# Optimization experiments

Hardware: AMD Instinct MI355X
Metric: run time of the kernel (lower is better)

The kernel has to match this reference:

```python
import jax, jax.numpy as jnp
import numpy as np

H = 2048      # hidden_size
NH = 16       # num_heads
HD = H // NH  # head_dim
B, T = 2, 2048


def setup_inputs() -> dict:
    key = jax.random.key(0)
    ks = jax.random.split(key, 5)
    s = 1.0 / np.sqrt(H)
    return {
        "x": jax.random.normal(ks[0], (B, T, H), dtype=jnp.float32),
        "wq": jax.random.normal(ks[1], (H, H), dtype=jnp.float32) * s,
        "bq": jnp.zeros((H,), dtype=jnp.float32),
        "wk": jax.random.normal(ks[2], (H, H), dtype=jnp.float32) * s,
        "bk": jnp.zeros((H,), dtype=jnp.float32),
        "wv": jax.random.normal(ks[3], (H, H), dtype=jnp.float32) * s,
        "bv": jnp.zeros((H,), dtype=jnp.float32),
        "wo": jax.random.normal(ks[4], (H, H), dtype=jnp.float32) * s,
        "bo": jnp.zeros((H,), dtype=jnp.float32),
    }


def reference(x, wq, bq, wk, bk, wv, bv, wo, bo):
    Bx, Tx, C = x.shape
    # projections (torch Linear: x @ W.T + b)
    q = x @ wq.T + bq
    k = x @ wk.T + bk
    v = x @ wv.T + bv
    # [B, T, H] -> [B, NH, T, HD]
    q = q.reshape(Bx, Tx, NH, HD).transpose(0, 2, 1, 3)
    k = k.reshape(Bx, Tx, NH, HD).transpose(0, 2, 1, 3)
    v = v.reshape(Bx, Tx, NH, HD).transpose(0, 2, 1, 3)
    scale = 1.0 / np.sqrt(HD).astype(np.float32)
    scores = jnp.einsum('bhqd,bhkd->bhqk', q, k) * scale  # [B, NH, T, T]
    causal = jnp.tril(jnp.ones((Tx, Tx), dtype=bool))
    scores = jnp.where(causal[None, None], scores, -jnp.inf)
    attn = jax.nn.softmax(scores, axis=-1)
    out = jnp.einsum('bhqk,bhkd->bhqd', attn, v)  # [B, NH, T, HD]
    out = out.transpose(0, 2, 1, 3).reshape(Bx, Tx, C)
    return out @ wo.T + bo
```

## Files before the change

### kernel.cpp

```cpp
#include <hip/hip_runtime.h>
#include <stdint.h>

constexpr int H_  = 2048;
constexpr int NH_ = 16;
constexpr int HD_ = 128;
constexpr int B_  = 2;
constexpr int T_  = 2048;
constexpr int M_  = B_ * T_;

typedef unsigned short u16;
typedef __bf16 bf16x8 __attribute__((ext_vector_type(8)));
typedef float  f32x4  __attribute__((ext_vector_type(4)));

constexpr float C1_ = 0.08838834764831845f * 1.4426950408889634f;

template <int N> struct IC { static constexpr int value = N; };

__device__ __forceinline__ u16 f2bf(float f) {
  uint32_t u = __builtin_bit_cast(uint32_t, f);
  u += 0x7fffu + ((u >> 16) & 1u);
  return (u16)(u >> 16);
}

__device__ __forceinline__ uint32_t cvtpk(float lo, float hi) {
  uint32_t r;
  asm("v_cvt_pk_bf16_f32 %0, %1, %2" : "=v"(r) : "v"(lo), "v"(hi));
  return r;
}

__device__ __forceinline__ void gload_lds16(const void* g, void* lds) {
  auto gp = (const __attribute__((address_space(1))) uint32_t*)(uintptr_t)g;
  auto lp = (__attribute__((address_space(3))) uint32_t*)(uint32_t)(uintptr_t)lds;
  __builtin_amdgcn_global_load_lds(gp, lp, 16, 0, 0);
}

__device__ __forceinline__ f32x4 mfma16(bf16x8 a, bf16x8 b, f32x4 c) {
  return __builtin_amdgcn_mfma_f32_16x16x32_bf16(a, b, c, 0, 0, 0);
}

__global__ __launch_bounds__(512) void cvt5_kernel(
    const float4* __restrict__ x,  const float4* __restrict__ wq,
    const float4* __restrict__ wk, const float4* __restrict__ wv,
    const float4* __restrict__ wo, ushort4* __restrict__ dst) {
  const int bid = blockIdx.x, tid = threadIdx.x;
  const float4* src;
  size_t idx, dof;
  if (bid < 4096) {
    src = x; idx = (size_t)bid * 512 + tid; dof = 0;
  } else {
    int w = (bid - 4096) >> 11;
    int r = (bid - 4096) & 2047;
    idx = (size_t)r * 512 + tid;
    dof = 2097152u + (size_t)w * 1048576u;
    src = (w == 0) ? wq : (w == 1) ? wk : (w == 2) ? wv : wo;
  }
  float4 v = src[idx];
  ushort4 o;
  o.x = f2bf(v.x); o.y = f2bf(v.y); o.z = f2bf(v.z); o.w = f2bf(v.w);
  dst[dof + idx] = o;
}

__device__ __forceinline__ void gemm_core(const u16* __restrict__ A,
                                          const u16* __restrict__ Bm,
                                          const float* __restrict__ bias,
                                          void* __restrict__ Cout,
                                          int bid, int outmode, float oscale) {
  __shared__ u16 As[2][128 * 64];
  __shared__ u16 Bs[2][128 * 64];
  constexpr int Mg = M_, Ng = H_, Kg = H_;
  const int tid = threadIdx.x;
  const int wave = tid >> 6, lane = tid & 63, l15 = lane & 15, lhi = lane >> 4;
  const int tm = bid % (Mg >> 7), tn = bid / (Mg >> 7);
  const int m0 = tm << 7, n0 = tn << 7;
  const int wr = wave >> 1, wc = wave & 1;
  const int NT = Kg >> 6;

  f32x4 acc[4][4] = {};

  auto stage = [&](int kt, int buf) {
#pragma unroll
    for (int is = 0; is < 4; ++is) {
      int o  = is * 4096 + tid * 16;
      int row = o >> 7;
      int sw  = o ^ (((o >> 7) & 7) << 4);
      int c8  = (sw >> 4) & 7;
      gload_lds16(A + (size_t)(m0 + row) * Kg + kt * 64 + c8 * 8,
                  &As[buf][0] + (is * 2048 + wave * 512));
      gload_lds16(Bm + (size_t)(n0 + row) * Kg + kt * 64 + c8 * 8,
                  &Bs[buf][0] + (is * 2048 + wave * 512));
    }
  };

  stage(0, 0);
  int cur = 0;
  for (int kt = 0; kt < NT; ++kt) {
    if (kt + 1 < NT) {
      stage(kt + 1, cur ^ 1);
      asm volatile("s_waitcnt vmcnt(8)" ::: "memory");
    } else {
      asm volatile("s_waitcnt vmcnt(0)" ::: "memory");
    }
    __builtin_amdgcn_s_barrier();
    asm volatile("" ::: "memory");
#pragma unroll
    for (int kk = 0; kk < 2; ++kk) {
      bf16x8 af[4], bfr[4];
#pragma unroll
      for (int mi = 0; mi < 4; ++mi) {
        int row = wr * 64 + mi * 16 + l15;
        int ob  = (row * 128 + kk * 64 + lhi * 16) ^ ((row & 7) << 4);
        af[mi] = *(const bf16x8*)((const char*)&As[cur][0] + ob);
      }
#pragma unroll
      for (int ni = 0; ni < 4; ++ni) {
        int row = wc * 64 + ni * 16 + l15;
        int ob  = (row * 128 + kk * 64 + lhi * 16) ^ ((row & 7) << 4);
        bfr[ni] = *(const bf16x8*)((const char*)&Bs[cur][0] + ob);
      }
#pragma unroll
      for (int mi = 0; mi < 4; ++mi)
#pragma unroll
        for (int ni = 0; ni < 4; ++ni)
          acc[mi][ni] = mfma16(af[mi], bfr[ni], acc[mi][ni]);
    }
    __builtin_amdgcn_s_barrier();
    asm volatile("" ::: "memory");
    cur ^= 1;
  }

  float bv[4];
#pragma unroll
  for (int ni = 0; ni < 4; ++ni) bv[ni] = bias[n0 + wc * 64 + ni * 16 + l15];

  if (outmode == 2) {
    const int b = m0 >> 11;
    const int tbase = (m0 & 2047) + wr * 64 + lhi * 4;
#pragma unroll
    for (int mi = 0; mi < 4; ++mi) {
#pragma unroll
      for (int ni = 0; ni < 4; ++ni) {
        int n = n0 + wc * 64 + ni * 16 + l15;
        ushort4 pk;
        pk.x = f2bf(acc[mi][ni][0] + bv[ni]);
        pk.y = f2bf(acc[mi][ni][1] + bv[ni]);
        pk.z = f2bf(acc[mi][ni][2] + bv[ni]);
        pk.w = f2bf(acc[mi][ni][3] + bv[ni]);
        *(ushort4*)((u16*)Cout + (size_t)(b * 2048 + n) * T_ + tbase +
                    mi * 16) = pk;
      }
    }
  } else {
#pragma unroll
    for (int mi = 0; mi < 4; ++mi) {
#pragma unroll
      for (int ni = 0; ni < 4; ++ni) {
        int n = n0 + wc * 64 + ni * 16 + l15;
#pragma unroll
        for (int r = 0; r < 4; ++r) {
          int m = m0 + wr * 64 + mi * 16 + lhi * 4 + r;
          float v = (acc[mi][ni][r] + bv[ni]) * oscale;
          if (outmode == 1)
            ((float*)Cout)[(size_t)m * Ng + n] = v;
          else
            ((u16*)Cout)[(size_t)m * Ng + n] = f2bf(v);
        }
      }
    }
  }
}

template <int OUTMODE>
__global__ __launch_bounds__(256) void gemm_bt_k(const u16* __restrict__ A,
                                                 const u16* __restrict__ Bm,
                                                 const float* __restrict__ bias,
                                                 void* __restrict__ Cout,
                                                 float oscale) {
  gemm_core(A, Bm, bias, Cout, blockIdx.x, OUTMODE, oscale);
}

__global__ __launch_bounds__(256, 2) void attn_kernel(
    const u16* __restrict__ Q, const u16* __restrict__ K,
    const u16* __restrict__ Vt, u16* __restrict__ ctx) {
  __shared__ u16 Ks[2][64 * 128];
  __shared__ u16 Vs[2][128 * 64];
  __shared__ u16 Ps[4][1024];

  const int tid = threadIdx.x, wave = tid >> 6, lane = tid & 63;
  const int l15 = lane & 15, lhi = lane >> 4;

  const int bid = blockIdx.x;
  const int xcd = bid & 7, idx = bid >> 3;
  const int bh = xcd * 4 + (idx & 3);
  const int qi = idx >> 2;
  const int b = bh >> 4, h = bh & 15;
  const int qb0 = qi, qb1 = 31 - qi;
  const int bt = qb0 + 1;

  const float THR = 11.5f;
  const float NI  = -__builtin_inff();

  auto stage = [&](auto bufc, int kv0) {
    constexpr int BUF = decltype(bufc)::value;
#pragma unroll
    for (int is = 0; is < 4; ++is) {
      {
        int o_ = is * 4096 + tid * 16;
        int row = o_ >> 8;
        int sw = o_ ^ (((o_ >> 8) & 7) << 4);
        int c8 = (sw >> 4) & 15;
        gload_lds16(K + (size_t)(b * T_ + kv0 + row) * H_ + h * HD_ + c8 * 8,
                    &Ks[BUF][0] + (is * 2048 + wave * 512));
      }
      {
        int o_ = is * 4096 + tid * 16;
        int row = o_ >> 7;
        int sw = o_ ^ (((o_ >> 7) & 7) << 4);
        int t8 = (sw >> 4) & 7;
        gload_lds16(Vt + (size_t)(bh * HD_ + row) * T_ + kv0 + t8 * 8,
                    &Vs[BUF][0] + (is * 4096 / 2 + wave * 512));
      }
    }
  };

  bf16x8 qc[4], qn[4];
  {
    const u16* q0p =
        Q + (size_t)(b * T_ + qb0 * 64 + wave * 16 + l15) * H_ + h * HD_ + lhi * 8;
    const u16* q1p =
        Q + (size_t)(b * T_ + qb1 * 64 + wave * 16 + l15) * H_ + h * HD_ + lhi * 8;
#pragma unroll
    for (int kk = 0; kk < 4; ++kk) {
      qc[kk] = *(const bf16x8*)(q0p + kk * 32);
      qn[kk] = *(const bf16x8*)(q1p + kk * 32);
    }
  }

  f32x4 o[8] = {};
  float m2 = NI, lr = 0.f;

  auto flushout = [&](int qtile) {
    float invo[4];
    float inv = 1.0f / lr;
#pragma unroll
    for (int r = 0; r < 4; ++r) invo[r] = __shfl(inv, lhi * 4 + r);
    int q0 = qtile * 64 + wave * 16;
#pragma unroll
    for (int dt = 0; dt < 8; ++dt)
#pragma unroll
      for (int r = 0; r < 4; ++r)
        ctx[(size_t)(b * T_ + q0 + lhi * 4 + r) * H_ + h * HD_ + dt * 16 +
            l15] = f2bf(o[dt][r] * invo[r]);
  };

  stage(IC<0>{}, 0);
  asm volatile("s_waitcnt vmcnt(0)" ::: "memory");
  __builtin_amdgcn_s_barrier();
  asm volatile("" ::: "memory");

  auto body = [&](int t, auto bufc) {
    constexpr int BUF = decltype(bufc)::value;
    if (t < 32) {
      int tn = t + 1;
      int kvn = ((tn >= bt) ? tn - bt : tn) * 64;
      stage(IC<BUF ^ 1>{}, kvn);
    }
    if (t == bt) {
      flushout(qb0);
#pragma unroll
      for (int dt = 0; dt < 8; ++dt) o[dt] = f32x4{0.f, 0.f, 0.f, 0.f};
      m2 = NI;
      lr = 0.f;
#pragma unroll
      for (int kk = 0; kk < 4; ++kk) qc[kk] = qn[kk];
    }
    if (t < 32)
      asm volatile("s_waitcnt vmcnt(8)" ::: "memory");
    else
      asm volatile("s_waitcnt vmcnt(0)" ::: "memory");
    __builtin_amdgcn_s_barrier();
    asm volatile("" ::: "memory");

    const int kvt = (t >= bt) ? t - bt : t;
    const int kv0 = kvt * 64;
    const int qtile = (t >= bt) ? qb1 : qb0;
    const int q0 = qtile * 64 + wave * 16;
    const int qrow = q0 + l15;

    f32x4 sv[4];
    __builtin_amdgcn_s_setprio(1);
#pragma unroll
    for (int kt = 0; kt < 4; ++kt) {
      f32x4 sacc = {0.f, 0.f, 0.f, 0.f};
#pragma unroll
      for (int kk = 0; kk < 4; ++kk) {
        int row = kt * 16 + l15;
        int ob = (row * 256 + kk * 64 + lhi * 16) ^ ((row & 7) << 4);
        bf16x8 kf = *(const bf16x8*)((const char*)&Ks[BUF][0] + ob);
        sacc = mfma16(kf, qc[kk], sacc);
      }
      sv[kt] = sacc;
    }
    __builtin_amdgcn_s_setprio(0);

    float pmax2 = NI;
    const bool diag = (t == qb0) || (t == 32);
    if (diag) {
#pragma unroll
      for (int kt = 0; kt < 4; ++kt)
#pragma unroll
        for (int r = 0; r < 4; ++r) {
          int key = kv0 + kt * 16 + lhi * 4 + r;
          float z = (key <= qrow) ? sv[kt][r] : NI;
          sv[kt][r] = z;
          pmax2 = fmaxf(pmax2, z);
        }
    } else {
#pragma unroll
      for (int kt = 0; kt < 4; ++kt)
#pragma unroll
        for (int r = 0; r < 4; ++r) pmax2 = fmaxf(pmax2, sv[kt][r]);
    }
    pmax2 = fmaxf(pmax2, __shfl_xor(pmax2, 16));
    pmax2 = fmaxf(pmax2, __shfl_xor(pmax2, 32));

    if (__any(pmax2 - m2 > THR)) {
      float mn = fmaxf(m2, pmax2);
      float al = exp2f(m2 - mn);
      m2 = mn;
      lr *= al;
      float alo[4];
#pragma unroll
      for (int r = 0; r < 4; ++r) alo[r] = __shfl(al, lhi * 4 + r);
#pragma unroll
      for (int dt = 0; dt < 8; ++dt)
#pragma unroll
        for (int r = 0; r < 4; ++r) o[dt][r] *= alo[r];
    }

    float rs = 0.f;
#pragma unroll
    for (int kt = 0; kt < 4; ++kt)
#pragma unroll
      for (int r = 0; r < 4; ++r) {
        float p = exp2f(sv[kt][r] - m2);
        sv[kt][r] = p;
        rs += p;
      }
    rs += __shfl_xor(rs, 16);
    rs += __shfl_xor(rs, 32);
    lr += rs;

#pragma unroll
    for (int kt = 0; kt < 4; ++kt) {
      int slot = kt * 2 + (lhi >> 1);
      uint2 pk;
      pk.x = cvtpk(sv[kt][0], sv[kt][1]);
      pk.y = cvtpk(sv[kt][2], sv[kt][3]);
      *(uint2*)&Ps[wave][slot * 128 + ((l15 * 8) ^ ((slot & 7) << 3)) +
                         (lhi & 1) * 4] = pk;
    }
    asm volatile("" ::: "memory");

    __builtin_amdgcn_s_setprio(1);
#pragma unroll
    for (int ks = 0; ks < 2; ++ks) {
      int slot = ks * 4 + lhi;
      bf16x8 pf = *(const bf16x8*)&Ps[wave][slot * 128 +
                                            ((l15 * 8) ^ ((slot & 7) << 3))];
#pragma unroll
      for (int dt = 0; dt < 8; ++dt) {
        int row = dt * 16 + l15;
        int ob = (row * 128 + ks * 64 + lhi * 16) ^ ((row & 7) << 4);
        bf16x8 vf = *(const bf16x8*)((const char*)&Vs[BUF][0] + ob);
        o[dt] = mfma16(pf, vf, o[dt]);
      }
    }
    __builtin_amdgcn_s_setprio(0);

    __builtin_amdgcn_s_barrier();
    asm volatile("" ::: "memory");
  };

#pragma unroll 1
  for (int t2 = 0; t2 < 32; t2 += 2) {
    body(t2, IC<0>{});
    body(t2 + 1, IC<1>{});
  }
  body(32, IC<0>{});
  flushout(qb1);
}

extern "C" void kernel_launch(void* const* d_in, const int* in_sizes, int n_in,
                              void* d_out, int out_size, void* d_ws,
                              size_t ws_size, hipStream_t stream) {
  const float* x  = (const float*)d_in[0];
  const float* wq = (const float*)d_in[1];
  const float* bq = (const float*)d_in[2];
  const float* wk = (const float*)d_in[3];
  const float* bk = (const float*)d_in[4];
  const float* wv = (const float*)d_in[5];
  const float* bv = (const float*)d_in[6];
  const float* wo = (const float*)d_in[7];
  const float* bo = (const float*)d_in[8];

  char* ws = (char*)d_ws;
  constexpr size_t SZ_X = (size_t)M_ * H_ * 2;
  constexpr size_t SZ_W = (size_t)H_ * H_ * 2;
  u16* xb  = (u16*)(ws);
  u16* wqb = (u16*)(ws + SZ_X);
  u16* wkb = (u16*)(ws + SZ_X + 1 * SZ_W);
  u16* wvb = (u16*)(ws + SZ_X + 2 * SZ_W);
  u16* wob = (u16*)(ws + SZ_X + 3 * SZ_W);
  u16* Qb  = (u16*)(ws + 1 * SZ_X + 4 * SZ_W);
  u16* Kb  = (u16*)(ws + 2 * SZ_X + 4 * SZ_W);
  u16* Vtb = (u16*)(ws + 3 * SZ_X + 4 * SZ_W);
  u16* ctx = xb;

  cvt5_kernel<<<12288, 512, 0, stream>>>((const float4*)x, (const float4*)wq,
                                         (const float4*)wk, (const float4*)wv,
                                         (const float4*)wo, (ushort4*)ws);

  gemm_bt_k<0><<<512, 256, 0, stream>>>(xb, wqb, bq, Qb, C1_);
  gemm_bt_k<0><<<512, 256, 0, stream>>>(xb, wkb, bk, Kb, 1.0f);
  gemm_bt_k<2><<<512, 256, 0, stream>>>(xb, wvb, bv, Vtb, 1.0f);

  attn_kernel<<<512, 256, 0, stream>>>(Qb, Kb, Vtb, ctx);

  gemm_bt_k<1><<<512, 256, 0, stream>>>(ctx, wob, bo, d_out, 1.0f);
}
```

Measured before the change: 250.0 us.

## Enlarge GEMM tiles to 256x128 with 8 waves and interleaved prefetch scheduling

Replaces the 128x128, 4-wave GEMM with a 256x128 tile computed by 8 waves per block. The next K-tile's global-to-LDS loads are split into chunks and interleaved between MFMA groups, with barriers and s_setprio raised around the MFMA bursts. The intent is more reuse of each loaded B tile and better overlap of memory loads with matrix math. In exchange, the larger LDS footprint (96KB per block) likely limits each CU to one block, and the grid becomes exactly 256 blocks.

```diff
diff --git a/kernel.cpp b/kernel.cpp
--- a/kernel.cpp
+++ b/kernel.cpp
@@ -60,71 +60,109 @@
   dst[dof + idx] = o;
 }
 
-__device__ __forceinline__ void gemm_core(const u16* __restrict__ A,
-                                          const u16* __restrict__ Bm,
-                                          const float* __restrict__ bias,
-                                          void* __restrict__ Cout,
-                                          int bid, int outmode, float oscale) {
-  __shared__ u16 As[2][128 * 64];
+__device__ __forceinline__ void gemm256_core(const u16* __restrict__ A,
+                                             const u16* __restrict__ Bm,
+                                             const float* __restrict__ bias,
+                                             void* __restrict__ Cout,
+                                             int bid, int outmode,
+                                             float oscale) {
+  __shared__ u16 As[2][256 * 64];
   __shared__ u16 Bs[2][128 * 64];
-  constexpr int Mg = M_, Ng = H_, Kg = H_;
+  constexpr int Kg = H_;
+  constexpr int NT = Kg / 64;
   const int tid = threadIdx.x;
   const int wave = tid >> 6, lane = tid & 63, l15 = lane & 15, lhi = lane >> 4;
-  const int tm = bid % (Mg >> 7), tn = bid / (Mg >> 7);
-  const int m0 = tm << 7, n0 = tn << 7;
+  const int tm = bid & 15, tn = bid >> 4;
+  const int m0 = tm << 8, n0 = tn << 7;
   const int wr = wave >> 1, wc = wave & 1;
-  const int NT = Kg >> 6;
 
   f32x4 acc[4][4] = {};
 
-  auto stage = [&](int kt, int buf) {
-#pragma unroll
-    for (int is = 0; is < 4; ++is) {
-      int o  = is * 4096 + tid * 16;
-      int row = o >> 7;
-      int sw  = o ^ (((o >> 7) & 7) << 4);
-      int c8  = (sw >> 4) & 7;
-      gload_lds16(A + (size_t)(m0 + row) * Kg + kt * 64 + c8 * 8,
-                  &As[buf][0] + (is * 2048 + wave * 512));
-      gload_lds16(Bm + (size_t)(n0 + row) * Kg + kt * 64 + c8 * 8,
-                  &Bs[buf][0] + (is * 2048 + wave * 512));
-    }
-  };
-
-  stage(0, 0);
+  auto stageA = [&](int kt, int buf, int a) {
+    int o = a * 8192 + tid * 16;
+    int row = o >> 7;
+    int sw = o ^ ((row & 7) << 4);
+    int c8 = (sw >> 4) & 7;
+    gload_lds16(A + (size_t)(m0 + row) * Kg + kt * 64 + c8 * 8,
+                (char*)&As[buf][0] + a * 8192 + wave * 1024);
+  };
+  auto stageB = [&](int kt, int buf, int a) {
+    int o = a * 8192 + tid * 16;
+    int row = o >> 7;
+    int sw = o ^ ((row & 7) << 4);
+    int c8 = (sw >> 4) & 7;
+    gload_lds16(Bm + (size_t)(n0 + row) * Kg + kt * 64 + c8 * 8,
+                (char*)&Bs[buf][0] + a * 8192 + wave * 1024);
+  };
+  auto rdA = [&](int buf, int kk, int mi) -> bf16x8 {
+    int row = wr * 64 + mi * 16 + l15;
+    int ob = (row * 128 + kk * 64 + lhi * 16) ^ ((row & 7) << 4);
+    return *(const bf16x8*)((const char*)&As[buf][0] + ob);
+  };
+  auto rdB = [&](int buf, int kk, int ni) -> bf16x8 {
+    int row = wc * 64 + ni * 16 + l15;
+    int ob = (row * 128 + kk * 64 + lhi * 16) ^ ((row & 7) << 4);
+    return *(const bf16x8*)((const char*)&Bs[buf][0] + ob);
+  };
+
+  stageB(0, 0, 0); stageB(0, 0, 1);
+  stageA(0, 0, 0); stageA(0, 0, 1); stageA(0, 0, 2); stageA(0, 0, 3);
+  asm volatile("s_waitcnt vmcnt(0)" ::: "memory");
+  __builtin_amdgcn_s_barrier();
+  asm volatile("" ::: "memory");
+
   int cur = 0;
   for (int kt = 0; kt < NT; ++kt) {
-    if (kt + 1 < NT) {
-      stage(kt + 1, cur ^ 1);
-      asm volatile("s_waitcnt vmcnt(8)" ::: "memory");
-    } else {
-      asm volatile("s_waitcnt vmcnt(0)" ::: "memory");
-    }
-    __builtin_amdgcn_s_barrier();
-    asm volatile("" ::: "memory");
-#pragma unroll
-    for (int kk = 0; kk < 2; ++kk) {
-      bf16x8 af[4], bfr[4];
-#pragma unroll
-      for (int mi = 0; mi < 4; ++mi) {
-        int row = wr * 64 + mi * 16 + l15;
-        int ob  = (row * 128 + kk * 64 + lhi * 16) ^ ((row & 7) << 4);
-        af[mi] = *(const bf16x8*)((const char*)&As[cur][0] + ob);
-      }
-#pragma unroll
-      for (int ni = 0; ni < 4; ++ni) {
-        int row = wc * 64 + ni * 16 + l15;
-        int ob  = (row * 128 + kk * 64 + lhi * 16) ^ ((row & 7) << 4);
-        bfr[ni] = *(const bf16x8*)((const char*)&Bs[cur][0] + ob);
-      }
-#pragma unroll
-      for (int mi = 0; mi < 4; ++mi)
-#pragma unroll
-        for (int ni = 0; ni < 4; ++ni)
-          acc[mi][ni] = mfma16(af[mi], bfr[ni], acc[mi][ni]);
-    }
-    __builtin_amdgcn_s_barrier();
-    asm volatile("" ::: "memory");
+    const bool hn = (kt + 1 < NT);
+    bf16x8 a0, a1, b0, b1, b2, b3;
+
+    a0 = rdA(cur, 0, 0); a1 = rdA(cur, 0, 1);
+    b0 = rdB(cur, 0, 0); b1 = rdB(cur, 0, 1);
+    b2 = rdB(cur, 0, 2); b3 = rdB(cur, 0, 3);
+    if (hn) { stageB(kt + 1, cur ^ 1, 0); stageB(kt + 1, cur ^ 1, 1); }
+    __builtin_amdgcn_s_barrier(); asm volatile("" ::: "memory");
+    __builtin_amdgcn_s_setprio(1);
+    acc[0][0] = mfma16(a0, b0, acc[0][0]); acc[0][1] = mfma16(a0, b1, acc[0][1]);
+    acc[0][2] = mfma16(a0, b2, acc[0][2]); acc[0][3] = mfma16(a0, b3, acc[0][3]);
+    acc[1][0] = mfma16(a1, b0, acc[1][0]); acc[1][1] = mfma16(a1, b1, acc[1][1]);
+    acc[1][2] = mfma16(a1, b2, acc[1][2]); acc[1][3] = mfma16(a1, b3, acc[1][3]);
+    __builtin_amdgcn_s_setprio(0);
+    __builtin_amdgcn_s_barrier(); asm volatile("" ::: "memory");
+
+    a0 = rdA(cur, 0, 2); a1 = rdA(cur, 0, 3);
+    if (hn) { stageA(kt + 1, cur ^ 1, 0); stageA(kt + 1, cur ^ 1, 1); }
+    __builtin_amdgcn_s_barrier(); asm volatile("" ::: "memory");
+    __builtin_amdgcn_s_setprio(1);
+    acc[2][0] = mfma16(a0, b0, acc[2][0]); acc[2][1] = mfma16(a0, b1, acc[2][1]);
+    acc[2][2] = mfma16(a0, b2, acc[2][2]); acc[2][3] = mfma16(a0, b3, acc[2][3]);
+    acc[3][0] = mfma16(a1, b0, acc[3][0]); acc[3][1] = mfma16(a1, b1, acc[3][1]);
+    acc[3][2] = mfma16(a1, b2, acc[3][2]); acc[3][3] = mfma16(a1, b3, acc[3][3]);
+    __builtin_amdgcn_s_setprio(0);
+    __builtin_amdgcn_s_barrier(); asm volatile("" ::: "memory");
+
+    a0 = rdA(cur, 1, 0); a1 = rdA(cur, 1, 1);
+    b0 = rdB(cur, 1, 0); b1 = rdB(cur, 1, 1);
+    b2 = rdB(cur, 1, 2); b3 = rdB(cur, 1, 3);
+    if (hn) { stageA(kt + 1, cur ^ 1, 2); stageA(kt + 1, cur ^ 1, 3); }
+    __builtin_amdgcn_s_barrier(); asm volatile("" ::: "memory");
+    __builtin_amdgcn_s_setprio(1);
+    acc[0][0] = mfma16(a0, b0, acc[0][0]); acc[0][1] = mfma16(a0, b1, acc[0][1]);
+    acc[0][2] = mfma16(a0, b2, acc[0][2]); acc[0][3] = mfma16(a0, b3, acc[0][3]);
+    acc[1][0] = mfma16(a1, b0, acc[1][0]); acc[1][1] = mfma16(a1, b1, acc[1][1]);
+    acc[1][2] = mfma16(a1, b2, acc[1][2]); acc[1][3] = mfma16(a1, b3, acc[1][3]);
+    __builtin_amdgcn_s_setprio(0);
+    __builtin_amdgcn_s_barrier(); asm volatile("" ::: "memory");
+
+    a0 = rdA(cur, 1, 2); a1 = rdA(cur, 1, 3);
+    __builtin_amdgcn_s_barrier(); asm volatile("" ::: "memory");
+    __builtin_amdgcn_s_setprio(1);
+    acc[2][0] = mfma16(a0, b0, acc[2][0]); acc[2][1] = mfma16(a0, b1, acc[2][1]);
+    acc[2][2] = mfma16(a0, b2, acc[2][2]); acc[2][3] = mfma16(a0, b3, acc[2][3]);
+    acc[3][0] = mfma16(a1, b0, acc[3][0]); acc[3][1] = mfma16(a1, b1, acc[3][1]);
+    acc[3][2] = mfma16(a1, b2, acc[3][2]); acc[3][3] = mfma16(a1, b3, acc[3][3]);
+    __builtin_amdgcn_s_setprio(0);
+    asm volatile("s_waitcnt vmcnt(0)" ::: "memory");
+    __builtin_amdgcn_s_barrier(); asm volatile("" ::: "memory");
     cur ^= 1;
   }
 
@@ -160,9 +198,9 @@
           int m = m0 + wr * 64 + mi * 16 + lhi * 4 + r;
           float v = (acc[mi][ni][r] + bv[ni]) * oscale;
           if (outmode == 1)
-            ((float*)Cout)[(size_t)m * Ng + n] = v;
+            ((float*)Cout)[(size_t)m * H_ + n] = v;
           else
-            ((u16*)Cout)[(size_t)m * Ng + n] = f2bf(v);
+            ((u16*)Cout)[(size_t)m * H_ + n] = f2bf(v);
         }
       }
     }
@@ -170,12 +208,10 @@
 }
 
 template <int OUTMODE>
-__global__ __launch_bounds__(256) void gemm_bt_k(const u16* __restrict__ A,
-                                                 const u16* __restrict__ Bm,
-                                                 const float* __restrict__ bias,
-                                                 void* __restrict__ Cout,
-                                                 float oscale) {
-  gemm_core(A, Bm, bias, Cout, blockIdx.x, OUTMODE, oscale);
+__global__ __launch_bounds__(512, 2) void gemm256_bt_k(
+    const u16* __restrict__ A, const u16* __restrict__ Bm,
+    const float* __restrict__ bias, void* __restrict__ Cout, float oscale) {
+  gemm256_core(A, Bm, bias, Cout, blockIdx.x, OUTMODE, oscale);
 }
 
 __global__ __launch_bounds__(256, 2) void attn_kernel(
@@ -420,11 +456,11 @@
                                          (const float4*)wk, (const float4*)wv,
                                          (const float4*)wo, (ushort4*)ws);
 
-  gemm_bt_k<0><<<512, 256, 0, stream>>>(xb, wqb, bq, Qb, C1_);
-  gemm_bt_k<0><<<512, 256, 0, stream>>>(xb, wkb, bk, Kb, 1.0f);
-  gemm_bt_k<2><<<512, 256, 0, stream>>>(xb, wvb, bv, Vtb, 1.0f);
+  gemm256_bt_k<0><<<256, 512, 0, stream>>>(xb, wqb, bq, Qb, C1_);
+  gemm256_bt_k<0><<<256, 512, 0, stream>>>(xb, wkb, bk, Kb, 1.0f);
+  gemm256_bt_k<2><<<256, 512, 0, stream>>>(xb, wvb, bv, Vtb, 1.0f);
 
   attn_kernel<<<512, 256, 0, stream>>>(Qb, Kb, Vtb, ctx);
 
-  gemm_bt_k<1><<<512, 256, 0, stream>>>(ctx, wob, bo, d_out, 1.0f);
-}
+  gemm256_bt_k<1><<<256, 512, 0, stream>>>(ctx, wob, bo, d_out, 1.0f);
+}
```

New measurement: 243.8 us. 2.5% less time.
